# Optimization experiments

Measured on AMD Instinct MI355X. Metric: run time of the kernel, lower is better.

## Reference

```python
import jax, jax.numpy as jnp
import numpy as np

RATIO, NH, NG, KS, RF, UP = 4, 2, 2, 3, 11.0, 2


def _cln(t, g, b):
    # channel-wise LayerNorm on NCHW (LayerNormProxy), eps=1e-5
    mu = t.mean(axis=1, keepdims=True)
    var = ((t - mu) ** 2).mean(axis=1, keepdims=True)
    return (t - mu) * jax.lax.rsqrt(var + 1e-5) * g[None, :, None, None] + b[None, :, None, None]


def _resize_ac(img, oH, oW):
    # bilinear resize, align_corners=True (F.interpolate)
    H, W = img.shape[-2], img.shape[-1]
    ys = jnp.arange(oH, dtype=img.dtype) * ((H - 1) / (oH - 1))
    y0 = jnp.clip(jnp.floor(ys), 0, H - 2).astype(jnp.int32)
    wy = ys - y0.astype(img.dtype)
    xs = jnp.arange(oW, dtype=img.dtype) * ((W - 1) / (oW - 1))
    x0 = jnp.clip(jnp.floor(xs), 0, W - 2).astype(jnp.int32)
    wx = xs - x0.astype(img.dtype)
    t = img[..., y0, :] * (1.0 - wy)[:, None] + img[..., y0 + 1, :] * wy[:, None]
    return t[..., x0] * (1.0 - wx) + t[..., x0 + 1] * wx


def _grid_sample(img, iy, ix):
    # bilinear grid_sample, padding_mode='zeros', align_corners=True
    # img [Bg,Cx,H,W]; iy,ix [Bg,N] unnormalized input-pixel coords
    H, W = img.shape[-2], img.shape[-1]
    def one(im, yy, xx):
        y0f, x0f = jnp.floor(yy), jnp.floor(xx)
        wy, wx = yy - y0f, xx - x0f
        y0, x0 = y0f.astype(jnp.int32), x0f.astype(jnp.int32)
        def gat(yi, xi):
            valid = ((yi >= 0) & (yi < H) & (xi >= 0) & (xi < W)).astype(im.dtype)
            return im[:, jnp.clip(yi, 0, H - 1), jnp.clip(xi, 0, W - 1)] * valid[None]
        return (gat(y0, x0) * ((1 - wy) * (1 - wx))[None]
                + gat(y0, x0 + 1) * ((1 - wy) * wx)[None]
                + gat(y0 + 1, x0) * (wy * (1 - wx))[None]
                + gat(y0 + 1, x0 + 1) * (wy * wx)[None])
    return jax.vmap(one)(img, iy, ix)


def _conv2d(x, w, groups=1):
    return jax.lax.conv_general_dilated(x, w, (1, 1), 'SAME', feature_group_count=groups,
                                        dimension_numbers=('NCHW', 'OIHW', 'NCHW'))


def _forward(x, ln_g, ln_b, Wq, Wk, dw_w, off_ln_g, off_ln_b, off_w, off_b, rpb):
    B, C, H, W = x.shape
    hidden = C // RATIO
    gc = hidden // NG
    c2 = hidden // NH          # attn_dim per head
    oH, oW = int(H * UP), int(W * UP)
    N1, n = oH * oW, KS * KS
    scale = c2 ** -0.5
    v = x
    xn = _cln(x, ln_g, ln_b)
    q = jnp.einsum('oc,bchw->bohw', Wq, xn)
    k = jnp.einsum('oc,bchw->bohw', Wk, xn)
    q = _resize_ac(q, oH, oW)                        # [B,hidden,oH,oW]
    # offset prediction
    q_off = q.reshape(B * NG, gc, oH, oW)
    t = _conv2d(q_off, dw_w, groups=gc)
    t = _cln(t, off_ln_g, off_ln_b)
    t = jax.nn.gelu(t, approximate=False)
    pred = _conv2d(t, off_w) + off_b[None, :, None, None]  # [Bg,2*ks^2,oH,oW]
    pad = (KS - 1) // 2
    rng = jnp.arange(-pad, pad + 1, dtype=x.dtype)
    base = jnp.stack(jnp.meshgrid(rng, rng, indexing='ij'), axis=-1)  # [KS,KS,2] (y,x)
    off = jnp.tanh(pred).reshape(B * NG, KS, KS, 2, oH, oW) * RF + base[None, :, :, :, None, None]
    py = off[:, :, :, 0] + jnp.arange(oH, dtype=x.dtype)[None, None, None, :, None]
    px = off[:, :, :, 1] + jnp.arange(oW, dtype=x.dtype)[None, None, None, None, :]
    # normalize over (oH-1,oW-1) then denormalize onto (H-1,W-1) input grid (align_corners)
    iy = (py * ((H - 1) / (oH - 1))).reshape(B * NG, -1)
    ix = (px * ((W - 1) / (oW - 1))).reshape(B * NG, -1)
    kg = k.reshape(B * NG, hidden // NG, H, W)
    vg = v.reshape(B * NG, C // NG, H, W)
    kf = _grid_sample(kg, iy, ix).reshape(B, NG, hidden // NG, n, oH, oW)
    vf = _grid_sample(vg, iy, ix).reshape(B, NG, C // NG, n, oH, oW)
    # -> [B, N1, n, g*c] -> [B, nh, N1, n, c]
    kf = kf.transpose(0, 4, 5, 3, 1, 2).reshape(B, N1, n, NH, hidden // NH).transpose(0, 3, 1, 2, 4)
    vf = vf.transpose(0, 4, 5, 3, 1, 2).reshape(B, N1, n, NH, C // NH).transpose(0, 3, 1, 2, 4)
    kf = kf + rpb                                     # relative position bias on K
    qh = q.reshape(B, NH, c2, N1).transpose(0, 1, 3, 2) * scale  # [B,nh,N1,c2]
    attn = jax.nn.softmax(jnp.einsum('bhnc,bhnkc->bhnk', qh, kf), axis=-1)
    out = jnp.einsum('bhnk,bhnkc->bhnc', attn, vf)    # [B,nh,N1,C/nh]
    return out.transpose(0, 1, 3, 2).reshape(B, C, oH, oW)


def setup_inputs() -> dict:
    key = jax.random.key(0)
    ks = jax.random.split(key, 8)
    B, C, H, W = 2, 256, 48, 48
    hidden = C // RATIO
    gc = hidden // NG
    c2 = hidden // NH
    f32 = jnp.float32
    return {
        'x': jax.random.normal(ks[0], (B, C, H, W), f32),
        'ln_g': jnp.ones((C,), f32),
        'ln_b': jnp.zeros((C,), f32),
        'Wq': jax.random.normal(ks[1], (hidden, C), f32) * 0.05,
        'Wk': jax.random.normal(ks[2], (hidden, C), f32) * 0.05,
        'dw_w': jax.random.normal(ks[3], (gc, 1, 3, 3), f32) * 0.1,
        'off_ln_g': jnp.ones((gc,), f32),
        'off_ln_b': jnp.zeros((gc,), f32),
        'off_w': jax.random.normal(ks[4], (2 * KS * KS, gc, 3, 3), f32) * 0.02,
        'off_b': jnp.zeros((2 * KS * KS,), f32),
        'rpb': jax.random.normal(ks[5], (1, NH, 1, KS * KS, c2), f32) * 0.02,
    }


def reference(x, ln_g, ln_b, Wq, Wk, dw_w, off_ln_g, off_ln_b, off_w, off_b, rpb):
    return _forward(x, ln_g, ln_b, Wq, Wk, dw_w, off_ln_g, off_ln_b, off_w, off_b, rpb)
```

## Files before the change

kernel.cpp:

```cpp
#include <hip/hip_runtime.h>
#include <hip/hip_fp16.h>
#include <cstdint>
#include <cmath>

#define NB 2
#define NC 256
#define HW 2304
#define HID 64
#define OH 96
#define OW 96
#define N1 9216
#define SCALE_ATTN 0.17677669529663689f
#define RESZ ((float)(47.0/95.0))

__device__ __host__ inline int ocb8(int w) { return w < 2 ? 3 * w : 6 + 2 * (w - 2); }
__device__ __host__ inline int cnt8(int w) { return w < 2 ? 3 : 2; }

struct h4v { __half2 lo, hi; };

__global__ void kA_prep(const float* __restrict__ x, const float* __restrict__ Wq,
                        const float* __restrict__ Wk, const float* __restrict__ off_w,
                        const float* __restrict__ dw_w, const float* __restrict__ off_b,
                        __half* __restrict__ v_nhwc, float* __restrict__ WT4,
                        float* __restrict__ dwT, float* __restrict__ wg2,
                        float* __restrict__ bsg2) {
    int blk = blockIdx.x;
    if (blk < 1152) {
        int pt = blk % 72;
        int t2 = blk / 72;
        int ct = t2 & 3;
        int bg = t2 >> 2;
        int b = bg >> 1, g = bg & 1;
        __shared__ float tile[32][33];
        int tx = threadIdx.x & 31, row = threadIdx.x >> 5;
#pragma unroll
        for (int r = 0; r < 4; r++) {
            int c = ct * 32 + row + r * 8;
            tile[row + r * 8][tx] = x[((size_t)(b * 256 + g * 128 + c)) * HW + pt * 32 + tx];
        }
        __syncthreads();
#pragma unroll
        for (int r = 0; r < 4; r++) {
            int p = pt * 32 + row + r * 8;
            v_nhwc[((size_t)bg * HW + p) * 128 + ct * 32 + tx] =
                __float2half(tile[tx][row + r * 8]);
        }
    } else {
        int idx = (blk - 1152) * 256 + threadIdx.x;
        if (idx < 32768) {
            int c = idx >> 7, t = idx & 127;
            float v = (t < 64) ? Wq[t * 256 + c] : Wk[(t - 64) * 256 + c];
            WT4[(((size_t)(c >> 2) * 128) + t) * 4 + (c & 3)] = v;
        } else if (idx < 32768 + 288) {
            int i = idx - 32768;
            int wi = i >> 5, c = i & 31;
            dwT[i] = dw_w[c * 9 + wi];
        } else if (idx < 32768 + 288 + 8 * 288 * 3) {
            int i = idx - (32768 + 288);
            int w = i / 864, r = i - w * 864;
            int kk = r / 3, j = r - kk * 3;
            wg2[i] = (j < cnt8(w)) ? off_w[(ocb8(w) + j) * 288 + kk] : 0.f;
        } else if (idx < 32768 + 288 + 8 * 288 * 3 + 24) {
            int i = idx - (32768 + 288 + 8 * 288 * 3);
            int w = i / 3, j = i - w * 3;
            bsg2[i] = (j < cnt8(w)) ? off_b[ocb8(w) + j] : 0.f;
        }
    }
}

__global__ __launch_bounds__(512) void k1_ln_qk(const __half* __restrict__ v_nhwc,
                         const float* __restrict__ ln_g, const float* __restrict__ ln_b,
                         const float* __restrict__ WT4,
                         float* __restrict__ q_pix, __half* __restrict__ k_nhwc) {
    int blk = blockIdx.x;
    int tid = threadIdx.x;
    int wv = tid >> 6, lane = tid & 63;
    __shared__ float xs[8][256];
    {
        int pix = blk * 8 + wv;
        int b = pix / HW, p = pix - b * HW;
        int c0 = lane * 2;
        __half2 h0 = *(const __half2*)(v_nhwc + (((size_t)(b * 2 + 0) * HW) + p) * 128 + c0);
        __half2 h1 = *(const __half2*)(v_nhwc + (((size_t)(b * 2 + 1) * HW) + p) * 128 + c0);
        float2 u0 = __half22float2(h0);
        float2 u1 = __half22float2(h1);
        float s = u0.x + u0.y + u1.x + u1.y;
#pragma unroll
        for (int off = 1; off < 64; off <<= 1) s += __shfl_xor(s, off);
        float mu = s * (1.f / 256.f);
        float d0 = u0.x - mu, d1 = u0.y - mu, d2 = u1.x - mu, d3 = u1.y - mu;
        float q = d0 * d0 + d1 * d1 + d2 * d2 + d3 * d3;
#pragma unroll
        for (int off = 1; off < 64; off <<= 1) q += __shfl_xor(q, off);
        float rs = rsqrtf(q * (1.f / 256.f) + 1e-5f);
        float2 w0, w1;
        w0.x = d0 * rs * ln_g[c0] + ln_b[c0];
        w0.y = d1 * rs * ln_g[c0 + 1] + ln_b[c0 + 1];
        w1.x = d2 * rs * ln_g[128 + c0] + ln_b[128 + c0];
        w1.y = d3 * rs * ln_g[129 + c0] + ln_b[129 + c0];
        *(float2*)&xs[wv][c0] = w0;
        *(float2*)&xs[wv][128 + c0] = w1;
    }
    __syncthreads();
    int o = tid & 127, ph = tid >> 7;
    float a0 = 0.f, a1 = 0.f;
    const float4* wp = (const float4*)WT4 + o;
    const float4* xa = (const float4*)xs[ph * 2];
    const float4* xb4 = (const float4*)xs[ph * 2 + 1];
#pragma unroll 8
    for (int c4 = 0; c4 < 64; c4++) {
        float4 w = wp[(size_t)c4 * 128];
        float4 p0 = xa[c4], p1 = xb4[c4];
        a0 += w.x * p0.x + w.y * p0.y + w.z * p0.z + w.w * p0.w;
        a1 += w.x * p1.x + w.y * p1.y + w.z * p1.z + w.w * p1.w;
    }
#pragma unroll
    for (int k = 0; k < 2; k++) {
        int pix = blk * 8 + ph * 2 + k;
        int b = pix / HW, p = pix - b * HW;
        float a = k ? a1 : a0;
        if (o < 64) {
            q_pix[(((size_t)b * HW) + p) * 64 + o] = a;
        } else {
            int t = o - 64, g = t >> 5, c32 = t & 31;
            k_nhwc[(((size_t)(b * 2 + g) * HW) + p) * 32 + c32] = __float2half(a);
        }
    }
}

__global__ __launch_bounds__(256) void k3_t(const float* __restrict__ q_pix,
                                            const float* __restrict__ dwT,
                                            const float* __restrict__ og,
                                            const float* __restrict__ ob,
                                            __half* __restrict__ tbuf_h) {
    int gid = blockIdx.x * 256 + threadIdx.x;
    int c = gid & 31;
    int p2 = gid >> 5;
    int bg = p2 / N1, p = p2 - bg * N1;
    int b = bg >> 1, g = bg & 1;
    int oy = p / OW, ox = p - oy * OW;
    const float* qb = q_pix + ((size_t)b * HW) * 64 + g * 32 + c;
    float acc = 0.f;
#pragma unroll
    for (int dy = -1; dy <= 1; dy++) {
        int yy = oy + dy;
        if ((unsigned)yy >= (unsigned)OH) continue;
        float ysf = yy * RESZ;
        int y0 = min((int)ysf, 46);
        float wy = ysf - (float)y0;
#pragma unroll
        for (int dx = -1; dx <= 1; dx++) {
            int xx = ox + dx;
            if ((unsigned)xx >= (unsigned)OW) continue;
            float xsf = xx * RESZ;
            int x0 = min((int)xsf, 46);
            float wx = xsf - (float)x0;
            int i00 = (y0 * 48 + x0) * 64;
            float q00 = qb[i00], q01 = qb[i00 + 64];
            float q10 = qb[i00 + 48 * 64], q11 = qb[i00 + 49 * 64];
            float qv = (q00 * (1.f - wy) + q10 * wy) * (1.f - wx)
                     + (q01 * (1.f - wy) + q11 * wy) * wx;
            acc += qv * dwT[((dy + 1) * 3 + dx + 1) * 32 + c];
        }
    }
    float s = acc;
#pragma unroll
    for (int off = 1; off < 32; off <<= 1) s += __shfl_xor(s, off);
    float mu = s * (1.f / 32.f);
    float d = acc - mu;
    float v = d * d;
#pragma unroll
    for (int off = 1; off < 32; off <<= 1) v += __shfl_xor(v, off);
    float rsv = rsqrtf(v * (1.f / 32.f) + 1e-5f);
    float t = d * rsv * og[c] + ob[c];
    float ge = 0.5f * t * (1.f + erff(t * 0.70710678118654752f));
    tbuf_h[(size_t)p2 * 32 + c] = __float2half(ge);
}

__global__ __launch_bounds__(512) void k4_pred(const __half* __restrict__ tbuf_h,
                                               const float* __restrict__ wg2,
                                               const float* __restrict__ bsg2,
                                               float* __restrict__ pred) {
    int blk = blockIdx.x;
    int bg = blk / 144, tile = blk - bg * 144;
    int ty0 = (tile / 12) * 8, tx0 = (tile % 12) * 8;
    int tid = threadIdx.x;
    __shared__ float ts[100 * 33];

    const __half* tb = tbuf_h + (size_t)bg * N1 * 32;
    for (int item = tid; item < 400; item += 512) {
        int pt = item >> 2, qg = item & 3;
        int hy = ty0 + pt / 10 - 1;
        int hx = tx0 + pt % 10 - 1;
        float4 raw = make_float4(0.f, 0.f, 0.f, 0.f);
        if ((unsigned)hy < (unsigned)OH && (unsigned)hx < (unsigned)OW)
            raw = *(const float4*)(tb + ((size_t)(hy * OW + hx)) * 32 + qg * 8);
        const __half2* h2 = (const __half2*)&raw;
        int base = pt * 33 + qg * 8;
#pragma unroll
        for (int i = 0; i < 4; i++) {
            float2 f = __half22float2(h2[i]);
            ts[base + i * 2] = f.x;
            ts[base + i * 2 + 1] = f.y;
        }
    }
    __syncthreads();

    int w = __builtin_amdgcn_readfirstlane(tid >> 6);
    int lane = tid & 63;
    int y = lane >> 3, x = lane & 7;
    int ocb = ocb8(w), cnt = cnt8(w);
    float acc[3];
#pragma unroll
    for (int j = 0; j < 3; j++) acc[j] = bsg2[w * 3 + j];
    const float* tsb = &ts[(y * 10 + x) * 33];
    const float* wgp = wg2 + (size_t)w * 864;
    const int kof[9] = {0, 33, 66, 330, 363, 396, 660, 693, 726};
    for (int ic = 0; ic < 32; ic++) {
#pragma unroll
        for (int k = 0; k < 9; k++) {
            float tv = tsb[kof[k] + ic];
            const float* wr = wgp + (ic * 9 + k) * 3;
#pragma unroll
            for (int j = 0; j < 3; j++) acc[j] += tv * wr[j];
        }
    }
    int p = (ty0 + y) * OW + tx0 + x;
    float* pp = pred + ((size_t)bg * N1 + p) * 18 + ocb;
#pragma unroll
    for (int j = 0; j < 3; j++)
        if (j < cnt) pp[j] = acc[j];
}

__global__ __launch_bounds__(256) void k5_attn(const float* __restrict__ pred,
                                               const float* __restrict__ q_pix,
                                               const __half* __restrict__ k_nhwc,
                                               const __half* __restrict__ v_nhwc,
                                               const float* __restrict__ rpb,
                                               float* __restrict__ out) {
    int tid = threadIdx.x;
    int wv = __builtin_amdgcn_readfirstlane(tid >> 6);
    int lane = tid & 63;
    int gp = blockIdx.x * 8;
    int bg = gp / N1, p0 = gp % N1;
    int b = bg >> 1, g = bg & 1;
    int pw = p0 + wv * 2;
    int oy = pw / OW, ox0 = pw % OW;

    __shared__ float4 wts[4][2][9];
    __shared__ int4   cof[4][2][9];
    __shared__ float  outb[4][2][128];

    if (lane < 18) {
        int px = lane / 9, j = lane % 9;
        int p = pw + px;
        int ky = j / 3, kx = j % 3;
        const float* pp = pred + ((size_t)bg * N1 + p) * 18;
        float pr0 = pp[j * 2];
        float pr1 = pp[j * 2 + 1];
        float th0 = 1.f - 2.f * __builtin_amdgcn_rcpf(__expf(2.f * pr0) + 1.f);
        float th1 = 1.f - 2.f * __builtin_amdgcn_rcpf(__expf(2.f * pr1) + 1.f);
        float py  = th0 * 11.0f + (float)(ky - 1) + (float)oy;
        float pxc = th1 * 11.0f + (float)(kx - 1) + (float)(ox0 + px);
        float iy = py * RESZ, ix = pxc * RESZ;
        float y0f = floorf(iy), x0f = floorf(ix);
        float wy = iy - y0f, wx = ix - x0f;
        int y0 = (int)y0f, x0 = (int)x0f;
        bool vy0 = (unsigned)y0 < 48u, vy1 = (unsigned)(y0 + 1) < 48u;
        bool vx0 = (unsigned)x0 < 48u, vx1 = (unsigned)(x0 + 1) < 48u;
        int y0c = min(max(y0, 0), 47), y1c = min(max(y0 + 1, 0), 47);
        int x0c = min(max(x0, 0), 47), x1c = min(max(x0 + 1, 0), 47);
        float4 w;
        w.x = (vy0 && vx0) ? (1.f - wy) * (1.f - wx) : 0.f;
        w.y = (vy0 && vx1) ? (1.f - wy) * wx : 0.f;
        w.z = (vy1 && vx0) ? wy * (1.f - wx) : 0.f;
        w.w = (vy1 && vx1) ? wy * wx : 0.f;
        wts[wv][px][j] = w;
        cof[wv][px][j] = make_int4(y0c * 48 + x0c, y0c * 48 + x1c,
                                   y1c * 48 + x0c, y1c * 48 + x1c);
    }
    __syncthreads();

    int c = lane & 31, h = lane >> 5;
    int c4 = (lane & 31) * 4;
    const __half* kb = k_nhwc + (size_t)bg * HW * 32;
    const float* rb = rpb + (size_t)g * 288;
    const float* qb = q_pix + (size_t)b * HW * 64 + g * 32 + c;
    const __half* vb = v_nhwc + (size_t)bg * HW * 128 + c4;

    float ysf = oy * RESZ;
    int qy0 = min((int)ysf, 46);
    float qwy = ysf - (float)qy0;

    float rv[5];
#pragma unroll
    for (int jj = 0; jj < 5; jj++) {
        int j = jj * 2 + h;
        rv[jj] = (j < 9) ? rb[j * 32 + c] : 0.f;
    }

    float qv[2];
#pragma unroll
    for (int px = 0; px < 2; px++) {
        float xsf = (ox0 + px) * RESZ;
        int qx0 = min((int)xsf, 46);
        float qwx = xsf - (float)qx0;
        int qi = (qy0 * 48 + qx0) * 64;
        float q00 = qb[qi], q01 = qb[qi + 64];
        float q10 = qb[qi + 48 * 64], q11 = qb[qi + 49 * 64];
        qv[px] = ((q00 * (1.f - qwy) + q10 * qwy) * (1.f - qwx)
                + (q01 * (1.f - qwy) + q11 * qwy) * qwx) * SCALE_ATTN;
    }

    float s[2][5];
#pragma unroll
    for (int px = 0; px < 2; px++) {
#pragma unroll
        for (int jj = 0; jj < 5; jj++) {
            int j = jj * 2 + h;
            float partial = 0.f;
            if (j < 9) {
                float4 w = wts[wv][px][j];
                int4 co = cof[wv][px][j];
                float kv = w.x * __half2float(kb[co.x * 32 + c])
                         + w.y * __half2float(kb[co.y * 32 + c])
                         + w.z * __half2float(kb[co.z * 32 + c])
                         + w.w * __half2float(kb[co.w * 32 + c]);
                partial = qv[px] * (kv + rv[jj]);
            }
#pragma unroll
            for (int off = 1; off < 32; off <<= 1) partial += __shfl_xor(partial, off);
            s[px][jj] = (j < 9) ? partial : -1e30f;
        }
    }

#pragma unroll
    for (int px = 0; px < 2; px++) {
        float m = s[px][0];
#pragma unroll
        for (int jj = 1; jj < 5; jj++) m = fmaxf(m, s[px][jj]);
        m = fmaxf(m, __shfl_xor(m, 32));
        float e[5];
        float sum = 0.f;
#pragma unroll
        for (int jj = 0; jj < 5; jj++) { e[jj] = __expf(s[px][jj] - m); sum += e[jj]; }
        sum += __shfl_xor(sum, 32);
        float inv = __builtin_amdgcn_rcpf(sum);
#pragma unroll
        for (int jj = 0; jj < 5; jj++) s[px][jj] = e[jj] * inv;
    }

    __half2 ac0[2], ac1[2];
#pragma unroll
    for (int px = 0; px < 2; px++) {
        ac0[px] = __float2half2_rn(0.f);
        ac1[px] = __float2half2_rn(0.f);
    }
#pragma unroll
    for (int px = 0; px < 2; px++) {
#pragma unroll
        for (int jj = 0; jj < 5; jj++) {
            int j = jj * 2 + h;
            if (j < 9) {
                float pj = s[px][jj];
                float4 w = wts[wv][px][j];
                int4 co = cof[wv][px][j];
                h4v a0 = *(const h4v*)(vb + (size_t)co.x * 128);
                h4v a1 = *(const h4v*)(vb + (size_t)co.y * 128);
                h4v a2 = *(const h4v*)(vb + (size_t)co.z * 128);
                h4v a3 = *(const h4v*)(vb + (size_t)co.w * 128);
                __half2 f0 = __float2half2_rn(w.x * pj);
                __half2 f1 = __float2half2_rn(w.y * pj);
                __half2 f2 = __float2half2_rn(w.z * pj);
                __half2 f3 = __float2half2_rn(w.w * pj);
                ac0[px] = __hfma2(f0, a0.lo, ac0[px]);
                ac1[px] = __hfma2(f0, a0.hi, ac1[px]);
                ac0[px] = __hfma2(f1, a1.lo, ac0[px]);
                ac1[px] = __hfma2(f1, a1.hi, ac1[px]);
                ac0[px] = __hfma2(f2, a2.lo, ac0[px]);
                ac1[px] = __hfma2(f2, a2.hi, ac1[px]);
                ac0[px] = __hfma2(f3, a3.lo, ac0[px]);
                ac1[px] = __hfma2(f3, a3.hi, ac1[px]);
            }
        }
    }
#pragma unroll
    for (int px = 0; px < 2; px++) {
        float2 lo = __half22float2(ac0[px]);
        float2 hi = __half22float2(ac1[px]);
        float4 acc = make_float4(lo.x, lo.y, hi.x, hi.y);
        acc.x += __shfl_xor(acc.x, 32);
        acc.y += __shfl_xor(acc.y, 32);
        acc.z += __shfl_xor(acc.z, 32);
        acc.w += __shfl_xor(acc.w, 32);
        if (lane < 32) *(float4*)&outb[wv][px][c4] = acc;
    }
    __syncthreads();

    {
        int ch = tid & 127, qh = tid >> 7;
        float* op = out + ((size_t)b * NC + g * 128 + ch) * N1 + p0 + qh * 4;
        float4 v4 = make_float4(outb[qh * 2][0][ch], outb[qh * 2][1][ch],
                                outb[qh * 2 + 1][0][ch], outb[qh * 2 + 1][1][ch]);
        *(float4*)op = v4;
    }
}

extern "C" void kernel_launch(void* const* d_in, const int* in_sizes, int n_in,
                              void* d_out, int out_size, void* d_ws, size_t ws_size,
                              hipStream_t stream) {
    const float* x      = (const float*)d_in[0];
    const float* ln_g   = (const float*)d_in[1];
    const float* ln_b   = (const float*)d_in[2];
    const float* Wq     = (const float*)d_in[3];
    const float* Wk     = (const float*)d_in[4];
    const float* dw_w   = (const float*)d_in[5];
    const float* off_g  = (const float*)d_in[6];
    const float* off_bt = (const float*)d_in[7];
    const float* off_w  = (const float*)d_in[8];
    const float* off_b  = (const float*)d_in[9];
    const float* rpb    = (const float*)d_in[10];
    float* out = (float*)d_out;

    float* ws = (float*)d_ws;
    float* WT4    = ws;
    float* q_pix  = WT4 + 32768;
    float* pred   = q_pix + 294912;
    float* dwT    = pred + 663552;
    float* wg2    = dwT + 288;
    float* bsg2   = wg2 + 6912;
    __half* v_nhwc = (__half*)(bsg2 + 24);
    __half* k_nhwc = v_nhwc + 1179648;
    __half* tbuf_h = k_nhwc + 294912;

    kA_prep<<<1309, 256, 0, stream>>>(x, Wq, Wk, off_w, dw_w, off_b,
                                      v_nhwc, WT4, dwT, wg2, bsg2);
    k1_ln_qk<<<576, 512, 0, stream>>>(v_nhwc, ln_g, ln_b, WT4, q_pix, k_nhwc);
    k3_t<<<4608, 256, 0, stream>>>(q_pix, dwT, off_g, off_bt, tbuf_h);
    k4_pred<<<576, 512, 0, stream>>>(tbuf_h, wg2, bsg2, pred);
    k5_attn<<<4608, 256, 0, stream>>>(pred, q_pix, k_nhwc, v_nhwc, rpb, out);
}
```

Measured before the change: 163.5 us.

## Move offset-to-sampling-weight computation into k4 and store upsampled q from k3

```diff
diff --git a/kernel.cpp b/kernel.cpp
--- a/kernel.cpp
+++ b/kernel.cpp
@@ -132,7 +132,8 @@
                                             const float* __restrict__ dwT,
                                             const float* __restrict__ og,
                                             const float* __restrict__ ob,
-                                            __half* __restrict__ tbuf_h) {
+                                            __half* __restrict__ tbuf_h,
+                                            float* __restrict__ qr) {
     int gid = blockIdx.x * 256 + threadIdx.x;
     int c = gid & 31;
     int p2 = gid >> 5;
@@ -141,6 +142,7 @@
     int oy = p / OW, ox = p - oy * OW;
     const float* qb = q_pix + ((size_t)b * HW) * 64 + g * 32 + c;
     float acc = 0.f;
+    float qcen = 0.f;
 #pragma unroll
     for (int dy = -1; dy <= 1; dy++) {
         int yy = oy + dy;
@@ -161,6 +163,7 @@
             float qv = (q00 * (1.f - wy) + q10 * wy) * (1.f - wx)
                      + (q01 * (1.f - wy) + q11 * wy) * wx;
             acc += qv * dwT[((dy + 1) * 3 + dx + 1) * 32 + c];
+            if (dy == 0 && dx == 0) qcen = qv;
         }
     }
     float s = acc;
@@ -175,17 +178,20 @@
     float t = d * rsv * og[c] + ob[c];
     float ge = 0.5f * t * (1.f + erff(t * 0.70710678118654752f));
     tbuf_h[(size_t)p2 * 32 + c] = __float2half(ge);
+    qr[((size_t)b * N1 + p) * 64 + g * 32 + c] = qcen;
 }
 
 __global__ __launch_bounds__(512) void k4_pred(const __half* __restrict__ tbuf_h,
                                                const float* __restrict__ wg2,
                                                const float* __restrict__ bsg2,
-                                               float* __restrict__ pred) {
+                                               float4* __restrict__ wtsg,
+                                               int4* __restrict__ cofg) {
     int blk = blockIdx.x;
     int bg = blk / 144, tile = blk - bg * 144;
     int ty0 = (tile / 12) * 8, tx0 = (tile % 12) * 8;
     int tid = threadIdx.x;
     __shared__ float ts[100 * 33];
+    __shared__ float ps[64][19];
 
     const __half* tb = tbuf_h + (size_t)bg * N1 * 32;
     for (int item = tid; item < 400; item += 512) {
@@ -206,62 +212,42 @@
     }
     __syncthreads();
 
-    int w = __builtin_amdgcn_readfirstlane(tid >> 6);
-    int lane = tid & 63;
-    int y = lane >> 3, x = lane & 7;
-    int ocb = ocb8(w), cnt = cnt8(w);
-    float acc[3];
-#pragma unroll
-    for (int j = 0; j < 3; j++) acc[j] = bsg2[w * 3 + j];
-    const float* tsb = &ts[(y * 10 + x) * 33];
-    const float* wgp = wg2 + (size_t)w * 864;
-    const int kof[9] = {0, 33, 66, 330, 363, 396, 660, 693, 726};
-    for (int ic = 0; ic < 32; ic++) {
-#pragma unroll
-        for (int k = 0; k < 9; k++) {
-            float tv = tsb[kof[k] + ic];
-            const float* wr = wgp + (ic * 9 + k) * 3;
-#pragma unroll
-            for (int j = 0; j < 3; j++) acc[j] += tv * wr[j];
-        }
-    }
-    int p = (ty0 + y) * OW + tx0 + x;
-    float* pp = pred + ((size_t)bg * N1 + p) * 18 + ocb;
-#pragma unroll
-    for (int j = 0; j < 3; j++)
-        if (j < cnt) pp[j] = acc[j];
-}
-
-__global__ __launch_bounds__(256) void k5_attn(const float* __restrict__ pred,
-                                               const float* __restrict__ q_pix,
-                                               const __half* __restrict__ k_nhwc,
-                                               const __half* __restrict__ v_nhwc,
-                                               const float* __restrict__ rpb,
-                                               float* __restrict__ out) {
-    int tid = threadIdx.x;
-    int wv = __builtin_amdgcn_readfirstlane(tid >> 6);
-    int lane = tid & 63;
-    int gp = blockIdx.x * 8;
-    int bg = gp / N1, p0 = gp % N1;
-    int b = bg >> 1, g = bg & 1;
-    int pw = p0 + wv * 2;
-    int oy = pw / OW, ox0 = pw % OW;
-
-    __shared__ float4 wts[4][2][9];
-    __shared__ int4   cof[4][2][9];
-    __shared__ float  outb[4][2][128];
-
-    if (lane < 18) {
-        int px = lane / 9, j = lane % 9;
-        int p = pw + px;
-        int ky = j / 3, kx = j % 3;
-        const float* pp = pred + ((size_t)bg * N1 + p) * 18;
-        float pr0 = pp[j * 2];
-        float pr1 = pp[j * 2 + 1];
+    {
+        int w = __builtin_amdgcn_readfirstlane(tid >> 6);
+        int lane = tid & 63;
+        int y = lane >> 3, x = lane & 7;
+        int ocb = ocb8(w), cnt = cnt8(w);
+        float acc[3];
+#pragma unroll
+        for (int j = 0; j < 3; j++) acc[j] = bsg2[w * 3 + j];
+        const float* tsb = &ts[(y * 10 + x) * 33];
+        const float* wgp = wg2 + (size_t)w * 864;
+        const int kof[9] = {0, 33, 66, 330, 363, 396, 660, 693, 726};
+        for (int ic = 0; ic < 32; ic++) {
+#pragma unroll
+            for (int k = 0; k < 9; k++) {
+                float tv = tsb[kof[k] + ic];
+                const float* wr = wgp + (ic * 9 + k) * 3;
+#pragma unroll
+                for (int j = 0; j < 3; j++) acc[j] += tv * wr[j];
+            }
+        }
+#pragma unroll
+        for (int j = 0; j < 3; j++)
+            if (j < cnt) ps[lane][ocb + j] = acc[j];
+    }
+    __syncthreads();
+
+    for (int item = tid; item < 576; item += 512) {
+        int pxl = item / 9, j = item - pxl * 9;
+        int oy = ty0 + (pxl >> 3), ox = tx0 + (pxl & 7);
+        int ky = j / 3, kx = j - ky * 3;
+        float pr0 = ps[pxl][2 * j];
+        float pr1 = ps[pxl][2 * j + 1];
         float th0 = 1.f - 2.f * __builtin_amdgcn_rcpf(__expf(2.f * pr0) + 1.f);
         float th1 = 1.f - 2.f * __builtin_amdgcn_rcpf(__expf(2.f * pr1) + 1.f);
         float py  = th0 * 11.0f + (float)(ky - 1) + (float)oy;
-        float pxc = th1 * 11.0f + (float)(kx - 1) + (float)(ox0 + px);
+        float pxc = th1 * 11.0f + (float)(kx - 1) + (float)ox;
         float iy = py * RESZ, ix = pxc * RESZ;
         float y0f = floorf(iy), x0f = floorf(ix);
         float wy = iy - y0f, wx = ix - x0f;
@@ -275,22 +261,37 @@
         w.y = (vy0 && vx1) ? (1.f - wy) * wx : 0.f;
         w.z = (vy1 && vx0) ? wy * (1.f - wx) : 0.f;
         w.w = (vy1 && vx1) ? wy * wx : 0.f;
-        wts[wv][px][j] = w;
-        cof[wv][px][j] = make_int4(y0c * 48 + x0c, y0c * 48 + x1c,
-                                   y1c * 48 + x0c, y1c * 48 + x1c);
-    }
-    __syncthreads();
+        size_t idx = ((size_t)bg * N1 + oy * OW + ox) * 9 + j;
+        wtsg[idx] = w;
+        cofg[idx] = make_int4(y0c * 48 + x0c, y0c * 48 + x1c,
+                              y1c * 48 + x0c, y1c * 48 + x1c);
+    }
+}
+
+__global__ __launch_bounds__(256) void k5_attn(const float4* __restrict__ wtsg,
+                                               const int4* __restrict__ cofg,
+                                               const float* __restrict__ qr,
+                                               const __half* __restrict__ k_nhwc,
+                                               const __half* __restrict__ v_nhwc,
+                                               const float* __restrict__ rpb,
+                                               float* __restrict__ out) {
+    int tid = threadIdx.x;
+    int wv = __builtin_amdgcn_readfirstlane(tid >> 6);
+    int lane = tid & 63;
+    int gp = blockIdx.x * 8;
+    int bg = gp / N1, p0 = gp % N1;
+    int b = bg >> 1, g = bg & 1;
+    int pw = p0 + wv * 2;
+
+    __shared__ float outb[4][2][128];
 
     int c = lane & 31, h = lane >> 5;
-    int c4 = (lane & 31) * 4;
+    int c4 = c * 4;
     const __half* kb = k_nhwc + (size_t)bg * HW * 32;
     const float* rb = rpb + (size_t)g * 288;
-    const float* qb = q_pix + (size_t)b * HW * 64 + g * 32 + c;
     const __half* vb = v_nhwc + (size_t)bg * HW * 128 + c4;
-
-    float ysf = oy * RESZ;
-    int qy0 = min((int)ysf, 46);
-    float qwy = ysf - (float)qy0;
+    const float4* wbase = wtsg + ((size_t)bg * N1 + pw) * 9;
+    const int4*   cbase = cofg + ((size_t)bg * N1 + pw) * 9;
 
     float rv[5];
 #pragma unroll
@@ -299,18 +300,10 @@
         rv[jj] = (j < 9) ? rb[j * 32 + c] : 0.f;
     }
 
+    const float* qrb = qr + ((size_t)b * N1 + pw) * 64 + g * 32 + c;
     float qv[2];
-#pragma unroll
-    for (int px = 0; px < 2; px++) {
-        float xsf = (ox0 + px) * RESZ;
-        int qx0 = min((int)xsf, 46);
-        float qwx = xsf - (float)qx0;
-        int qi = (qy0 * 48 + qx0) * 64;
-        float q00 = qb[qi], q01 = qb[qi + 64];
-        float q10 = qb[qi + 48 * 64], q11 = qb[qi + 49 * 64];
-        qv[px] = ((q00 * (1.f - qwy) + q10 * qwy) * (1.f - qwx)
-                + (q01 * (1.f - qwy) + q11 * qwy) * qwx) * SCALE_ATTN;
-    }
+    qv[0] = qrb[0] * SCALE_ATTN;
+    qv[1] = qrb[64] * SCALE_ATTN;
 
     float s[2][5];
 #pragma unroll
@@ -320,8 +313,8 @@
             int j = jj * 2 + h;
             float partial = 0.f;
             if (j < 9) {
-                float4 w = wts[wv][px][j];
-                int4 co = cof[wv][px][j];
+                float4 w = wbase[px * 9 + j];
+                int4 co = cbase[px * 9 + j];
                 float kv = w.x * __half2float(kb[co.x * 32 + c])
                          + w.y * __half2float(kb[co.y * 32 + c])
                          + w.z * __half2float(kb[co.z * 32 + c])
@@ -363,8 +356,8 @@
             int j = jj * 2 + h;
             if (j < 9) {
                 float pj = s[px][jj];
-                float4 w = wts[wv][px][j];
-                int4 co = cof[wv][px][j];
+                float4 w = wbase[px * 9 + j];
+                int4 co = cbase[px * 9 + j];
                 h4v a0 = *(const h4v*)(vb + (size_t)co.x * 128);
                 h4v a1 = *(const h4v*)(vb + (size_t)co.y * 128);
                 h4v a2 = *(const h4v*)(vb + (size_t)co.z * 128);
@@ -425,18 +418,20 @@
     float* ws = (float*)d_ws;
     float* WT4    = ws;
     float* q_pix  = WT4 + 32768;
-    float* pred   = q_pix + 294912;
-    float* dwT    = pred + 663552;
+    float* dwT    = q_pix + 294912;
     float* wg2    = dwT + 288;
     float* bsg2   = wg2 + 6912;
-    __half* v_nhwc = (__half*)(bsg2 + 24);
+    float* qr     = bsg2 + 24;
+    float4* wtsg  = (float4*)(qr + 1179648);
+    int4*   cofg  = (int4*)(wtsg + 331776);
+    __half* v_nhwc = (__half*)(cofg + 331776);
     __half* k_nhwc = v_nhwc + 1179648;
     __half* tbuf_h = k_nhwc + 294912;
 
     kA_prep<<<1309, 256, 0, stream>>>(x, Wq, Wk, off_w, dw_w, off_b,
                                       v_nhwc, WT4, dwT, wg2, bsg2);
     k1_ln_qk<<<576, 512, 0, stream>>>(v_nhwc, ln_g, ln_b, WT4, q_pix, k_nhwc);
-    k3_t<<<4608, 256, 0, stream>>>(q_pix, dwT, off_g, off_bt, tbuf_h);
-    k4_pred<<<576, 512, 0, stream>>>(tbuf_h, wg2, bsg2, pred);
-    k5_attn<<<4608, 256, 0, stream>>>(pred, q_pix, k_nhwc, v_nhwc, rpb, out);
-}
+    k3_t<<<4608, 256, 0, stream>>>(q_pix, dwT, off_g, off_bt, tbuf_h, qr);
+    k4_pred<<<576, 512, 0, stream>>>(tbuf_h, wg2, bsg2, wtsg, cofg);
+    k5_attn<<<4608, 256, 0, stream>>>(wtsg, cofg, qr, k_nhwc, v_nhwc, rpb, out);
+}
```

Measured after the change: 181.1 us. +10.7%, slower.

## Reuse upsampled q from offset kernel and widen attention lane work per sample

Applied to the files above, without the earlier changes.

```diff
diff --git a/kernel.cpp b/kernel.cpp
--- a/kernel.cpp
+++ b/kernel.cpp
@@ -15,8 +15,6 @@
 
 __device__ __host__ inline int ocb8(int w) { return w < 2 ? 3 * w : 6 + 2 * (w - 2); }
 __device__ __host__ inline int cnt8(int w) { return w < 2 ? 3 : 2; }
-
-struct h4v { __half2 lo, hi; };
 
 __global__ void kA_prep(const float* __restrict__ x, const float* __restrict__ Wq,
                         const float* __restrict__ Wk, const float* __restrict__ off_w,
@@ -132,7 +130,8 @@
                                             const float* __restrict__ dwT,
                                             const float* __restrict__ og,
                                             const float* __restrict__ ob,
-                                            __half* __restrict__ tbuf_h) {
+                                            __half* __restrict__ tbuf_h,
+                                            float* __restrict__ qr) {
     int gid = blockIdx.x * 256 + threadIdx.x;
     int c = gid & 31;
     int p2 = gid >> 5;
@@ -141,6 +140,7 @@
     int oy = p / OW, ox = p - oy * OW;
     const float* qb = q_pix + ((size_t)b * HW) * 64 + g * 32 + c;
     float acc = 0.f;
+    float qcen = 0.f;
 #pragma unroll
     for (int dy = -1; dy <= 1; dy++) {
         int yy = oy + dy;
@@ -161,6 +161,7 @@
             float qv = (q00 * (1.f - wy) + q10 * wy) * (1.f - wx)
                      + (q01 * (1.f - wy) + q11 * wy) * wx;
             acc += qv * dwT[((dy + 1) * 3 + dx + 1) * 32 + c];
+            if (dy == 0 && dx == 0) qcen = qv;
         }
     }
     float s = acc;
@@ -175,6 +176,7 @@
     float t = d * rsv * og[c] + ob[c];
     float ge = 0.5f * t * (1.f + erff(t * 0.70710678118654752f));
     tbuf_h[(size_t)p2 * 32 + c] = __float2half(ge);
+    qr[((size_t)b * N1 + p) * 64 + g * 32 + c] = qcen;
 }
 
 __global__ __launch_bounds__(512) void k4_pred(const __half* __restrict__ tbuf_h,
@@ -233,7 +235,7 @@
 }
 
 __global__ __launch_bounds__(256) void k5_attn(const float* __restrict__ pred,
-                                               const float* __restrict__ q_pix,
+                                               const float* __restrict__ qr,
                                                const __half* __restrict__ k_nhwc,
                                                const __half* __restrict__ v_nhwc,
                                                const float* __restrict__ rpb,
@@ -281,119 +283,122 @@
     }
     __syncthreads();
 
-    int c = lane & 31, h = lane >> 5;
-    int c4 = (lane & 31) * 4;
-    const __half* kb = k_nhwc + (size_t)bg * HW * 32;
+    int c2 = lane & 15, jg = lane >> 4;
+    const __half* kb = k_nhwc + (size_t)bg * HW * 32 + 2 * c2;
     const float* rb = rpb + (size_t)g * 288;
-    const float* qb = q_pix + (size_t)b * HW * 64 + g * 32 + c;
-    const __half* vb = v_nhwc + (size_t)bg * HW * 128 + c4;
-
-    float ysf = oy * RESZ;
-    int qy0 = min((int)ysf, 46);
-    float qwy = ysf - (float)qy0;
-
-    float rv[5];
-#pragma unroll
-    for (int jj = 0; jj < 5; jj++) {
-        int j = jj * 2 + h;
-        rv[jj] = (j < 9) ? rb[j * 32 + c] : 0.f;
-    }
-
-    float qv[2];
+    const __half* vb = v_nhwc + (size_t)bg * HW * 128 + c2 * 8;
+
+    float2 rv[3];
+#pragma unroll
+    for (int jj = 0; jj < 3; jj++) {
+        int j = jj * 4 + jg;
+        rv[jj] = (j < 9) ? *(const float2*)(rb + j * 32 + 2 * c2) : make_float2(0.f, 0.f);
+    }
+
+    const float* qrb = qr + ((size_t)b * N1 + pw) * 64 + g * 32 + 2 * c2;
+    float2 qv[2];
+    {
+        float2 t0 = *(const float2*)qrb;
+        float2 t1 = *(const float2*)(qrb + 64);
+        qv[0] = make_float2(t0.x * SCALE_ATTN, t0.y * SCALE_ATTN);
+        qv[1] = make_float2(t1.x * SCALE_ATTN, t1.y * SCALE_ATTN);
+    }
+
+    float s[2][3];
 #pragma unroll
     for (int px = 0; px < 2; px++) {
-        float xsf = (ox0 + px) * RESZ;
-        int qx0 = min((int)xsf, 46);
-        float qwx = xsf - (float)qx0;
-        int qi = (qy0 * 48 + qx0) * 64;
-        float q00 = qb[qi], q01 = qb[qi + 64];
-        float q10 = qb[qi + 48 * 64], q11 = qb[qi + 49 * 64];
-        qv[px] = ((q00 * (1.f - qwy) + q10 * qwy) * (1.f - qwx)
-                + (q01 * (1.f - qwy) + q11 * qwy) * qwx) * SCALE_ATTN;
-    }
-
-    float s[2][5];
-#pragma unroll
-    for (int px = 0; px < 2; px++) {
-#pragma unroll
-        for (int jj = 0; jj < 5; jj++) {
-            int j = jj * 2 + h;
+#pragma unroll
+        for (int jj = 0; jj < 3; jj++) {
+            int j = jj * 4 + jg;
             float partial = 0.f;
             if (j < 9) {
                 float4 w = wts[wv][px][j];
                 int4 co = cof[wv][px][j];
-                float kv = w.x * __half2float(kb[co.x * 32 + c])
-                         + w.y * __half2float(kb[co.y * 32 + c])
-                         + w.z * __half2float(kb[co.z * 32 + c])
-                         + w.w * __half2float(kb[co.w * 32 + c]);
-                partial = qv[px] * (kv + rv[jj]);
+                float2 k0 = __half22float2(*(const __half2*)(kb + (size_t)co.x * 32));
+                float2 k1 = __half22float2(*(const __half2*)(kb + (size_t)co.y * 32));
+                float2 k2 = __half22float2(*(const __half2*)(kb + (size_t)co.z * 32));
+                float2 k3 = __half22float2(*(const __half2*)(kb + (size_t)co.w * 32));
+                float kvx = w.x * k0.x + w.y * k1.x + w.z * k2.x + w.w * k3.x;
+                float kvy = w.x * k0.y + w.y * k1.y + w.z * k2.y + w.w * k3.y;
+                partial = qv[px].x * (kvx + rv[jj].x) + qv[px].y * (kvy + rv[jj].y);
             }
 #pragma unroll
-            for (int off = 1; off < 32; off <<= 1) partial += __shfl_xor(partial, off);
+            for (int off = 1; off < 16; off <<= 1) partial += __shfl_xor(partial, off);
             s[px][jj] = (j < 9) ? partial : -1e30f;
         }
     }
 
+    float pj[2][3];
 #pragma unroll
     for (int px = 0; px < 2; px++) {
-        float m = s[px][0];
-#pragma unroll
-        for (int jj = 1; jj < 5; jj++) m = fmaxf(m, s[px][jj]);
+        float m = fmaxf(fmaxf(s[px][0], s[px][1]), s[px][2]);
+        m = fmaxf(m, __shfl_xor(m, 16));
         m = fmaxf(m, __shfl_xor(m, 32));
-        float e[5];
-        float sum = 0.f;
-#pragma unroll
-        for (int jj = 0; jj < 5; jj++) { e[jj] = __expf(s[px][jj] - m); sum += e[jj]; }
+        float e0 = __expf(s[px][0] - m);
+        float e1 = __expf(s[px][1] - m);
+        float e2 = __expf(s[px][2] - m);
+        float sum = e0 + e1 + e2;
+        sum += __shfl_xor(sum, 16);
         sum += __shfl_xor(sum, 32);
         float inv = __builtin_amdgcn_rcpf(sum);
-#pragma unroll
-        for (int jj = 0; jj < 5; jj++) s[px][jj] = e[jj] * inv;
-    }
-
-    __half2 ac0[2], ac1[2];
+        pj[px][0] = e0 * inv; pj[px][1] = e1 * inv; pj[px][2] = e2 * inv;
+    }
+
+    __half2 acc[2][4];
+#pragma unroll
+    for (int px = 0; px < 2; px++)
+#pragma unroll
+        for (int q = 0; q < 4; q++) acc[px][q] = __float2half2_rn(0.f);
+
 #pragma unroll
     for (int px = 0; px < 2; px++) {
-        ac0[px] = __float2half2_rn(0.f);
-        ac1[px] = __float2half2_rn(0.f);
-    }
-#pragma unroll
-    for (int px = 0; px < 2; px++) {
-#pragma unroll
-        for (int jj = 0; jj < 5; jj++) {
-            int j = jj * 2 + h;
+#pragma unroll
+        for (int jj = 0; jj < 3; jj++) {
+            int j = jj * 4 + jg;
             if (j < 9) {
-                float pj = s[px][jj];
+                float p = pj[px][jj];
                 float4 w = wts[wv][px][j];
                 int4 co = cof[wv][px][j];
-                h4v a0 = *(const h4v*)(vb + (size_t)co.x * 128);
-                h4v a1 = *(const h4v*)(vb + (size_t)co.y * 128);
-                h4v a2 = *(const h4v*)(vb + (size_t)co.z * 128);
-                h4v a3 = *(const h4v*)(vb + (size_t)co.w * 128);
-                __half2 f0 = __float2half2_rn(w.x * pj);
-                __half2 f1 = __float2half2_rn(w.y * pj);
-                __half2 f2 = __float2half2_rn(w.z * pj);
-                __half2 f3 = __float2half2_rn(w.w * pj);
-                ac0[px] = __hfma2(f0, a0.lo, ac0[px]);
-                ac1[px] = __hfma2(f0, a0.hi, ac1[px]);
-                ac0[px] = __hfma2(f1, a1.lo, ac0[px]);
-                ac1[px] = __hfma2(f1, a1.hi, ac1[px]);
-                ac0[px] = __hfma2(f2, a2.lo, ac0[px]);
-                ac1[px] = __hfma2(f2, a2.hi, ac1[px]);
-                ac0[px] = __hfma2(f3, a3.lo, ac0[px]);
-                ac1[px] = __hfma2(f3, a3.hi, ac1[px]);
+                float4 r0 = *(const float4*)(vb + (size_t)co.x * 128);
+                float4 r1 = *(const float4*)(vb + (size_t)co.y * 128);
+                float4 r2 = *(const float4*)(vb + (size_t)co.z * 128);
+                float4 r3 = *(const float4*)(vb + (size_t)co.w * 128);
+                const __half2* A0 = (const __half2*)&r0;
+                const __half2* A1 = (const __half2*)&r1;
+                const __half2* A2 = (const __half2*)&r2;
+                const __half2* A3 = (const __half2*)&r3;
+                __half2 f0 = __float2half2_rn(w.x * p);
+                __half2 f1 = __float2half2_rn(w.y * p);
+                __half2 f2 = __float2half2_rn(w.z * p);
+                __half2 f3 = __float2half2_rn(w.w * p);
+#pragma unroll
+                for (int q = 0; q < 4; q++) {
+                    acc[px][q] = __hfma2(f0, A0[q], acc[px][q]);
+                    acc[px][q] = __hfma2(f1, A1[q], acc[px][q]);
+                    acc[px][q] = __hfma2(f2, A2[q], acc[px][q]);
+                    acc[px][q] = __hfma2(f3, A3[q], acc[px][q]);
+                }
             }
         }
     }
+
 #pragma unroll
     for (int px = 0; px < 2; px++) {
-        float2 lo = __half22float2(ac0[px]);
-        float2 hi = __half22float2(ac1[px]);
-        float4 acc = make_float4(lo.x, lo.y, hi.x, hi.y);
-        acc.x += __shfl_xor(acc.x, 32);
-        acc.y += __shfl_xor(acc.y, 32);
-        acc.z += __shfl_xor(acc.z, 32);
-        acc.w += __shfl_xor(acc.w, 32);
-        if (lane < 32) *(float4*)&outb[wv][px][c4] = acc;
+        float f[8];
+#pragma unroll
+        for (int q = 0; q < 4; q++) {
+            float2 t = __half22float2(acc[px][q]);
+            f[2 * q] = t.x; f[2 * q + 1] = t.y;
+        }
+#pragma unroll
+        for (int i = 0; i < 8; i++) {
+            f[i] += __shfl_xor(f[i], 16);
+            f[i] += __shfl_xor(f[i], 32);
+        }
+        if (lane < 16) {
+            *(float4*)&outb[wv][px][c2 * 8]     = make_float4(f[0], f[1], f[2], f[3]);
+            *(float4*)&outb[wv][px][c2 * 8 + 4] = make_float4(f[4], f[5], f[6], f[7]);
+        }
     }
     __syncthreads();
 
@@ -432,11 +437,12 @@
     __half* v_nhwc = (__half*)(bsg2 + 24);
     __half* k_nhwc = v_nhwc + 1179648;
     __half* tbuf_h = k_nhwc + 294912;
+    float* qr      = (float*)(tbuf_h + 1179648);
 
     kA_prep<<<1309, 256, 0, stream>>>(x, Wq, Wk, off_w, dw_w, off_b,
                                       v_nhwc, WT4, dwT, wg2, bsg2);
     k1_ln_qk<<<576, 512, 0, stream>>>(v_nhwc, ln_g, ln_b, WT4, q_pix, k_nhwc);
-    k3_t<<<4608, 256, 0, stream>>>(q_pix, dwT, off_g, off_bt, tbuf_h);
+    k3_t<<<4608, 256, 0, stream>>>(q_pix, dwT, off_g, off_bt, tbuf_h, qr);
     k4_pred<<<576, 512, 0, stream>>>(tbuf_h, wg2, bsg2, pred);
-    k5_attn<<<4608, 256, 0, stream>>>(pred, q_pix, k_nhwc, v_nhwc, rpb, out);
-}
+    k5_attn<<<4608, 256, 0, stream>>>(pred, qr, k_nhwc, v_nhwc, rpb, out);
+}
```

Measured after the change: 155.6 us. -4.9%, faster.
